# Kernel tuning notes

Hardware: AMD Instinct MI355X
Metric: run time of the kernel (lower is better)

## Reference

```python
import jax, jax.numpy as jnp
import numpy as np

USER_COUNT = 100000
ITEM_COUNT = 100000
DIM = 64
B = 1024
NPOS = 10
NTOP = 50
CLAMP = 40.0
EPS = 1e-05


def setup_inputs() -> dict:
    key = jax.random.key(0)
    k1, k2, k3, k4, k5 = jax.random.split(key, 5)
    user_emb = jax.random.normal(k1, (USER_COUNT, DIM), dtype=jnp.float32) * 0.01
    item_emb = jax.random.normal(k2, (ITEM_COUNT, DIM), dtype=jnp.float32) * 0.01
    batch_user = jax.random.randint(k3, (B,), 0, USER_COUNT)
    pos_items = jax.random.randint(k4, (B, NPOS), 0, ITEM_COUNT)
    top_items = jax.random.randint(k5, (B, NTOP), 0, ITEM_COUNT)
    batch_user_mask = jnp.zeros((B, ITEM_COUNT), dtype=jnp.float32)
    return {
        "user_emb": user_emb,
        "item_emb": item_emb,
        "batch_user": batch_user,
        "pos_items": pos_items,
        "top_items": top_items,
        "batch_user_mask": batch_user_mask,
        "is_final": 1,
    }


def _overall_loss(mat, pos_items, top_items, mask):
    # tops: scores at pos+top indices, [B, NPOS+NTOP]
    tops = jnp.take_along_axis(mat, jnp.concatenate([pos_items, top_items], -1), axis=1)
    tops_els = (jnp.exp(mat) * (1.0 - mask)).sum(1, keepdims=True)  # [B,1]
    els = tops_els - jnp.exp(jnp.take_along_axis(mat, top_items, axis=1)).sum(1, keepdims=True)
    above = tops.reshape(-1, 1)
    below = jnp.broadcast_to(els, (els.shape[0], tops.shape[1])).reshape(-1, 1) + jnp.exp(above)
    below = jnp.log(jnp.clip(below, EPS))
    return -(above - below).sum()


def _rank_loss(mat, pos_items, top_items, mask):
    S_pos = jnp.take_along_axis(mat, pos_items, axis=1)                       # [B,NPOS]
    S_top = jnp.take_along_axis(mat, top_items[:, : NTOP // 2], axis=1)       # [B,NTOP/2]
    exp_masked_sum = (jnp.exp(mat) * (1.0 - mask)).sum(1, keepdims=True)      # [B,1]
    below2 = exp_masked_sum - jnp.exp(S_top).sum(1, keepdims=True)
    above_pos = S_pos.sum(1, keepdims=True)
    above_top = S_top.sum(1, keepdims=True)
    below_pos = jnp.cumsum(jnp.exp(jnp.flip(S_pos, -1)), axis=1)
    below_top = jnp.cumsum(jnp.exp(jnp.flip(S_top, -1)), axis=1)
    below_pos = jnp.log(jnp.clip(below_pos + below2, EPS)).sum(1, keepdims=True)
    below_top = jnp.log(jnp.clip(below_top + below2, EPS)).sum(1, keepdims=True)
    pos_KD_loss = -(above_pos - below_pos).sum()
    S_top_sub = jnp.take_along_axis(mat, top_items[:, : NTOP // 10], axis=1)  # [B,NTOP/10]
    below2_sub = exp_masked_sum - jnp.exp(S_top_sub).sum(1, keepdims=True)
    above_top_sub = S_top_sub.sum(1, keepdims=True)
    below_top_sub = jnp.cumsum(jnp.exp(jnp.flip(S_top_sub, -1)), axis=1)
    below_top_sub = jnp.log(jnp.clip(below_top_sub + below2_sub, EPS)).sum(1, keepdims=True)
    top_KD_loss = -(above_top - below_top).sum() - (above_top_sub - below_top_sub).sum()
    return pos_KD_loss + top_KD_loss / 2


def reference(user_emb, item_emb, batch_user, pos_items, top_items, batch_user_mask, is_final):
    u = user_emb[batch_user]                                  # [B, DIM]
    mat = jnp.clip(u @ item_emb.T, -CLAMP, CLAMP)             # [B, ITEM_COUNT]
    if is_final:
        return _rank_loss(mat, pos_items, top_items, batch_user_mask)
    return _overall_loss(mat, pos_items, top_items, batch_user_mask)
```

## Files before the change

### kernel.cpp

```cpp
#include <hip/hip_runtime.h>
#include <cstddef>
#include <cstdint>

#define USER_COUNT_C 100000
#define ITEM_COUNT_C 100000
#define DIM_C 64
#define B_C 1024
#define NPOS_C 10
#define NTOP_C 50
#define CLAMP_C 40.0f
#define EPS_C 1e-5f

#define NGROUPS 6250
#define NCHUNKS 3125
#define GX 48
#define GY 16

using bf16x8 = __attribute__((ext_vector_type(8))) short;
using f32x4  = __attribute__((ext_vector_type(4))) float;

__global__ void zero_ws_kernel(float* __restrict__ ws) {
    ws[threadIdx.x] = 0.0f;
}

__device__ inline short f2bf(float x) {
    uint32_t b = __float_as_uint(x);
    uint32_t r = (b + 0x7fffu + ((b >> 16) & 1u)) >> 16;
    return (short)r;
}

__device__ inline bf16x8 cvt8(const float* __restrict__ p) {
    float4 v0 = *(const float4*)p;
    float4 v1 = *(const float4*)(p + 4);
    bf16x8 r;
    r[0] = f2bf(v0.x); r[1] = f2bf(v0.y); r[2] = f2bf(v0.z); r[3] = f2bf(v0.w);
    r[4] = f2bf(v1.x); r[5] = f2bf(v1.y); r[6] = f2bf(v1.z); r[7] = f2bf(v1.w);
    return r;
}

__global__ __launch_bounds__(256) void prep_items_kernel(
    const float* __restrict__ item_emb, short* __restrict__ item_bf16) {
    const int t = blockIdx.x * 256 + threadIdx.x;
    const int n16 = t & 15;
    const int q   = (t >> 4) & 3;
    const int h   = (t >> 6) & 1;
    const int g   = t >> 7;
    const int i   = g * 16 + n16;
    bf16x8 v = cvt8(item_emb + (size_t)i * DIM_C + h * 32 + q * 8);
    *(bf16x8*)(item_bf16 + (((size_t)g * 2 + h) * 4 + q) * 128 + n16 * 8) = v;
}

__global__ __launch_bounds__(256, 3) void expsum_mfma5_kernel(
    const float* __restrict__ user_emb,
    const short* __restrict__ item_bf16,
    const int*   __restrict__ batch_user,
    const float* __restrict__ mask,
    float*       __restrict__ exp_sum)
{
    const int tid  = threadIdx.x;
    const int wave = tid >> 6;
    const int lane = tid & 63;
    const int n16  = lane & 15;
    const int quad = lane >> 4;
    const int uBase = blockIdx.y * 64;

    bf16x8 b0[4], b1[4];
    #pragma unroll
    for (int j = 0; j < 4; ++j) {
        const int uidx = batch_user[uBase + j * 16 + n16];
        const float* us = user_emb + (size_t)uidx * DIM_C + quad * 8;
        b0[j] = cvt8(us);
        b1[j] = cvt8(us + 32);
    }

    const float* mbase = mask + (size_t)(uBase + n16) * ITEM_COUNT_C;
    const short* fbase = item_bf16 + quad * 128 + n16 * 8;

    const int c0 = (int)(((long)blockIdx.x * NCHUNKS) / GX);
    const int c1 = (int)(((long)(blockIdx.x + 1) * NCHUNKS) / GX);

    float accE[4] = {0.f, 0.f, 0.f, 0.f};

    for (int c = c0 + wave; c < c1; c += 4) {
        float4 m[4][2];
        #pragma unroll
        for (int j = 0; j < 4; ++j)
            #pragma unroll
            for (int ig = 0; ig < 2; ++ig)
                m[j][ig] = *(const float4*)(mbase + (size_t)j * 16 * ITEM_COUNT_C
                                            + c * 32 + ig * 16 + quad * 4);

        const short* fp = fbase + (size_t)c * 2048;
        const bf16x8 a00 = *(const bf16x8*)fp;
        const bf16x8 a01 = *(const bf16x8*)(fp + 512);
        const bf16x8 a10 = *(const bf16x8*)(fp + 1024);
        const bf16x8 a11 = *(const bf16x8*)(fp + 1536);

        f32x4 acc[2][4];
        #pragma unroll
        for (int j = 0; j < 4; ++j) {
            acc[0][j] = (f32x4){0.f, 0.f, 0.f, 0.f};
            acc[0][j] = __builtin_amdgcn_mfma_f32_16x16x32_bf16(a00, b0[j], acc[0][j], 0, 0, 0);
            acc[0][j] = __builtin_amdgcn_mfma_f32_16x16x32_bf16(a01, b1[j], acc[0][j], 0, 0, 0);
            acc[1][j] = (f32x4){0.f, 0.f, 0.f, 0.f};
            acc[1][j] = __builtin_amdgcn_mfma_f32_16x16x32_bf16(a10, b0[j], acc[1][j], 0, 0, 0);
            acc[1][j] = __builtin_amdgcn_mfma_f32_16x16x32_bf16(a11, b1[j], acc[1][j], 0, 0, 0);
        }

        #pragma unroll
        for (int j = 0; j < 4; ++j)
            #pragma unroll
            for (int ig = 0; ig < 2; ++ig) {
                const float* mp = (const float*)&m[j][ig];
                #pragma unroll
                for (int r = 0; r < 4; ++r) {
                    const float sc = fminf(fmaxf(acc[ig][j][r], -CLAMP_C), CLAMP_C);
                    accE[j] += __expf(sc) * (1.0f - mp[r]);
                }
            }
    }

    #pragma unroll
    for (int j = 0; j < 4; ++j) {
        accE[j] += __shfl_xor(accE[j], 16, 64);
        accE[j] += __shfl_xor(accE[j], 32, 64);
    }
    if (quad == 0) {
        #pragma unroll
        for (int j = 0; j < 4; ++j)
            atomicAdd(&exp_sum[uBase + j * 16 + n16], accE[j]);
    }
}

__global__ __launch_bounds__(256) void expsum_fallback_kernel(
    const float* __restrict__ user_emb,
    const float* __restrict__ item_emb,
    const int*   __restrict__ batch_user,
    const float* __restrict__ mask,
    float*       __restrict__ exp_sum)
{
    const int tid  = threadIdx.x;
    const int wave = tid >> 6;
    const int lane = tid & 63;
    const int n16  = lane & 15;
    const int quad = lane >> 4;
    const int rowBase = blockIdx.y * 64 + wave * 16;

    const int uidx = batch_user[rowBase + n16];
    const float* usrc = user_emb + (size_t)uidx * DIM_C + quad * 8;
    const bf16x8 a0 = cvt8(usrc);
    const bf16x8 a1 = cvt8(usrc + 32);

    float accExp[4] = {0.f, 0.f, 0.f, 0.f};

    for (int t = blockIdx.x; t < NGROUPS / 4; t += 64) {
        const int ibase = t * 64;
        bf16x8 b0[4], b1[4];
        #pragma unroll
        for (int s = 0; s < 4; ++s) {
            const int gi = ibase + s * 16 + n16;
            const float* isrc = item_emb + (size_t)gi * DIM_C + quad * 8;
            b0[s] = cvt8(isrc);
            b1[s] = cvt8(isrc + 32);
        }
        f32x4 acc[4];
        #pragma unroll
        for (int s = 0; s < 4; ++s) {
            acc[s] = (f32x4){0.f, 0.f, 0.f, 0.f};
            acc[s] = __builtin_amdgcn_mfma_f32_16x16x32_bf16(a0, b0[s], acc[s], 0, 0, 0);
            acc[s] = __builtin_amdgcn_mfma_f32_16x16x32_bf16(a1, b1[s], acc[s], 0, 0, 0);
        }
        #pragma unroll
        for (int s = 0; s < 4; ++s)
            #pragma unroll
            for (int reg = 0; reg < 4; ++reg) {
                const int row = rowBase + quad * 4 + reg;
                const float sc = fminf(fmaxf(acc[s][reg], -CLAMP_C), CLAMP_C);
                const float w = 1.0f - mask[(size_t)row * ITEM_COUNT_C + ibase + s * 16 + n16];
                accExp[reg] += __expf(sc) * w;
            }
    }
    #pragma unroll
    for (int off = 1; off < 16; off <<= 1)
        #pragma unroll
        for (int reg = 0; reg < 4; ++reg)
            accExp[reg] += __shfl_xor(accExp[reg], off, 64);
    if (n16 == 0)
        #pragma unroll
        for (int reg = 0; reg < 4; ++reg)
            atomicAdd(&exp_sum[rowBase + quad * 4 + reg], accExp[reg]);
}

__global__ void finalize_kernel(
    const float* __restrict__ user_emb,
    const float* __restrict__ item_emb,
    const int*   __restrict__ batch_user,
    const int*   __restrict__ pos_items,
    const int*   __restrict__ top_items,
    const float* __restrict__ exp_sum,
    const int*   __restrict__ is_final,
    float*       __restrict__ row_loss)
{
    __shared__ float ush[DIM_C];
    __shared__ float s_sh[NPOS_C + NTOP_C];
    const int b = blockIdx.x;
    const int tid = threadIdx.x;
    const int uidx = batch_user[b];
    if (tid < 16)
        *(float4*)&ush[tid * 4] = *(const float4*)(user_emb + (size_t)uidx * DIM_C + tid * 4);
    __syncthreads();

    if (tid < NPOS_C + NTOP_C) {
        const int idx = (tid < NPOS_C) ? pos_items[b * NPOS_C + tid]
                                       : top_items[b * NTOP_C + (tid - NPOS_C)];
        const float* iv = item_emb + (size_t)idx * DIM_C;
        float s = 0.f;
        #pragma unroll
        for (int d4 = 0; d4 < 16; ++d4) {
            const float4 a = *(const float4*)(iv + d4 * 4);
            s += a.x * ush[d4 * 4 + 0] + a.y * ush[d4 * 4 + 1]
               + a.z * ush[d4 * 4 + 2] + a.w * ush[d4 * 4 + 3];
        }
        s_sh[tid] = fminf(fmaxf(s, -CLAMP_C), CLAMP_C);
    }
    __syncthreads();

    if (tid == 0) {
        const float E = exp_sum[b];
        float L;
        if (is_final[0] != 0) {
            float sumExpTop = 0.f, above_top = 0.f;
            for (int i = 0; i < NTOP_C / 2; ++i) {
                const float v = s_sh[NPOS_C + i];
                sumExpTop += __expf(v); above_top += v;
            }
            const float below2 = E - sumExpTop;
            float above_pos = 0.f;
            for (int i = 0; i < NPOS_C; ++i) above_pos += s_sh[i];
            float c = 0.f, below_pos = 0.f;
            for (int i = 0; i < NPOS_C; ++i) {
                c += __expf(s_sh[NPOS_C - 1 - i]);
                below_pos += __logf(fmaxf(c + below2, EPS_C));
            }
            float c2 = 0.f, below_top = 0.f;
            for (int i = 0; i < NTOP_C / 2; ++i) {
                c2 += __expf(s_sh[NPOS_C + NTOP_C / 2 - 1 - i]);
                below_top += __logf(fmaxf(c2 + below2, EPS_C));
            }
            const float pos_KD = below_pos - above_pos;
            float sumExpSub = 0.f, above_sub = 0.f;
            for (int i = 0; i < NTOP_C / 10; ++i) {
                const float v = s_sh[NPOS_C + i];
                sumExpSub += __expf(v); above_sub += v;
            }
            const float below2s = E - sumExpSub;
            float c3 = 0.f, below_sub = 0.f;
            for (int i = 0; i < NTOP_C / 10; ++i) {
                c3 += __expf(s_sh[NPOS_C + NTOP_C / 10 - 1 - i]);
                below_sub += __logf(fmaxf(c3 + below2s, EPS_C));
            }
            const float top_KD = (below_top - above_top) + (below_sub - above_sub);
            L = pos_KD + 0.5f * top_KD;
        } else {
            float sumExpTop = 0.f;
            for (int i = 0; i < NTOP_C; ++i) sumExpTop += __expf(s_sh[NPOS_C + i]);
            const float els = E - sumExpTop;
            L = 0.f;
            for (int j = 0; j < NPOS_C + NTOP_C; ++j) {
                const float a = s_sh[j];
                L += __logf(fmaxf(els + __expf(a), EPS_C)) - a;
            }
        }
        row_loss[b] = L;
    }
}

__global__ void reduce_kernel(const float* __restrict__ rl, float* __restrict__ out) {
    __shared__ float part[16];
    const int tid = threadIdx.x;
    float v = rl[tid];
    #pragma unroll
    for (int off = 32; off > 0; off >>= 1) v += __shfl_down(v, off, 64);
    if ((tid & 63) == 0) part[tid >> 6] = v;
    __syncthreads();
    if (tid == 0) {
        float s = 0.f;
        #pragma unroll
        for (int i = 0; i < 16; ++i) s += part[i];
        out[0] = s;
    }
}

extern "C" void kernel_launch(void* const* d_in, const int* in_sizes, int n_in,
                              void* d_out, int out_size, void* d_ws, size_t ws_size,
                              hipStream_t stream) {
    const float* user_emb   = (const float*)d_in[0];
    const float* item_emb   = (const float*)d_in[1];
    const int*   batch_user = (const int*)d_in[2];
    const int*   pos_items  = (const int*)d_in[3];
    const int*   top_items  = (const int*)d_in[4];
    const float* mask       = (const float*)d_in[5];
    const int*   is_final   = (const int*)d_in[6];
    float* out = (float*)d_out;

    float* exp_sum  = (float*)d_ws;
    float* row_loss = exp_sum + B_C;
    short* item_bf16 = (short*)(row_loss + B_C);
    const size_t need = 2 * B_C * sizeof(float)
                      + (size_t)NGROUPS * 1024 * sizeof(short);

    hipLaunchKernelGGL(zero_ws_kernel, dim3(1), dim3(B_C), 0, stream, exp_sum);
    if (ws_size >= need) {
        hipLaunchKernelGGL(prep_items_kernel, dim3(NGROUPS * 128 / 256), dim3(256),
                           0, stream, item_emb, item_bf16);
        hipLaunchKernelGGL(expsum_mfma5_kernel, dim3(GX, GY), dim3(256),
                           0, stream, user_emb, item_bf16, batch_user, mask, exp_sum);
    } else {
        hipLaunchKernelGGL(expsum_fallback_kernel, dim3(64, B_C / 64), dim3(256),
                           0, stream, user_emb, item_emb, batch_user, mask, exp_sum);
    }
    hipLaunchKernelGGL(finalize_kernel, dim3(B_C), dim3(64), 0, stream,
                       user_emb, item_emb, batch_user, pos_items, top_items,
                       exp_sum, is_final, row_loss);
    hipLaunchKernelGGL(reduce_kernel, dim3(1), dim3(B_C), 0, stream, row_loss, out);
}
```

Before: 593.2 us.

## Stage mask tiles through shared memory with row-contiguous coalesced loads

Restructures the exp-sum kernel so each block handles 128-item tiles. All 256 threads cooperatively load a 64x128 mask tile into LDS using contiguous 512-byte row segments, and the waves then read their mask values from LDS. Previously each wave loaded scattered 128-byte row pieces for 16 users straight into registers. The goal is better coalescing on the dominant 400 MB mask read, at the cost of two barriers per tile, no double buffering, and a padded tail tile that reads extra zero-weighted item groups.

```diff
diff --git a/kernel.cpp b/kernel.cpp
--- a/kernel.cpp
+++ b/kernel.cpp
@@ -12,9 +12,10 @@
 #define EPS_C 1e-5f
 
 #define NGROUPS 6250
-#define NCHUNKS 3125
+#define T_TILES 782
 #define GX 48
 #define GY 16
+#define MROW 132
 
 using bf16x8 = __attribute__((ext_vector_type(8))) short;
 using f32x4  = __attribute__((ext_vector_type(4))) float;
@@ -47,16 +48,18 @@
     const int g   = t >> 7;
     const int i   = g * 16 + n16;
     bf16x8 v = cvt8(item_emb + (size_t)i * DIM_C + h * 32 + q * 8);
-    *(bf16x8*)(item_bf16 + (((size_t)g * 2 + h) * 4 + q) * 128 + n16 * 8) = v;
-}
-
-__global__ __launch_bounds__(256, 3) void expsum_mfma5_kernel(
+    *(bf16x8*)(item_bf16 + (size_t)g * 1024 + h * 512 + q * 128 + n16 * 8) = v;
+}
+
+__global__ __launch_bounds__(256, 3) void expsum_mfma6_kernel(
     const float* __restrict__ user_emb,
     const short* __restrict__ item_bf16,
     const int*   __restrict__ batch_user,
     const float* __restrict__ mask,
     float*       __restrict__ exp_sum)
 {
+    __shared__ float mtile[64 * MROW];
+
     const int tid  = threadIdx.x;
     const int wave = tid >> 6;
     const int lane = tid & 63;
@@ -73,24 +76,30 @@
         b1[j] = cvt8(us + 32);
     }
 
-    const float* mbase = mask + (size_t)(uBase + n16) * ITEM_COUNT_C;
-    const short* fbase = item_bf16 + quad * 128 + n16 * 8;
-
-    const int c0 = (int)(((long)blockIdx.x * NCHUNKS) / GX);
-    const int c1 = (int)(((long)(blockIdx.x + 1) * NCHUNKS) / GX);
+    const int srow = tid >> 5;
+    const int scol = (tid & 31) * 4;
+    const float* smask = mask + (size_t)(uBase + srow) * ITEM_COUNT_C + scol;
+    float* sdst = &mtile[srow * MROW + scol];
 
     float accE[4] = {0.f, 0.f, 0.f, 0.f};
 
-    for (int c = c0 + wave; c < c1; c += 4) {
-        float4 m[4][2];
-        #pragma unroll
-        for (int j = 0; j < 4; ++j)
-            #pragma unroll
-            for (int ig = 0; ig < 2; ++ig)
-                m[j][ig] = *(const float4*)(mbase + (size_t)j * 16 * ITEM_COUNT_C
-                                            + c * 32 + ig * 16 + quad * 4);
-
-        const short* fp = fbase + (size_t)c * 2048;
+    for (int tile = blockIdx.x; tile < T_TILES; tile += GX) {
+        const int C = tile * 128;
+
+        #pragma unroll
+        for (int k = 0; k < 8; ++k) {
+            const int gitem = C + scol;
+            float4 v;
+            if (gitem < ITEM_COUNT_C)
+                v = *(const float4*)(smask + (size_t)(k * 8) * ITEM_COUNT_C + C);
+            else
+                v = make_float4(1.f, 1.f, 1.f, 1.f);
+            *(float4*)(sdst + k * 8 * MROW) = v;
+        }
+        __syncthreads();
+
+        const short* fp = item_bf16 + (size_t)(tile * 8 + wave * 2) * 1024
+                        + quad * 128 + n16 * 8;
         const bf16x8 a00 = *(const bf16x8*)fp;
         const bf16x8 a01 = *(const bf16x8*)(fp + 512);
         const bf16x8 a10 = *(const bf16x8*)(fp + 1024);
@@ -108,16 +117,20 @@
         }
 
         #pragma unroll
-        for (int j = 0; j < 4; ++j)
+        for (int j = 0; j < 4; ++j) {
             #pragma unroll
             for (int ig = 0; ig < 2; ++ig) {
-                const float* mp = (const float*)&m[j][ig];
+                const int l = wave * 32 + ig * 16 + quad * 4;
+                const float4 mv = *(const float4*)&mtile[(j * 16 + n16) * MROW + l];
+                const float* mp = (const float*)&mv;
                 #pragma unroll
                 for (int r = 0; r < 4; ++r) {
                     const float sc = fminf(fmaxf(acc[ig][j][r], -CLAMP_C), CLAMP_C);
                     accE[j] += __expf(sc) * (1.0f - mp[r]);
                 }
             }
+        }
+        __syncthreads();
     }
 
     #pragma unroll
@@ -307,13 +320,13 @@
     float* row_loss = exp_sum + B_C;
     short* item_bf16 = (short*)(row_loss + B_C);
     const size_t need = 2 * B_C * sizeof(float)
-                      + (size_t)NGROUPS * 1024 * sizeof(short);
+                      + ((size_t)NGROUPS + 16) * 1024 * sizeof(short);
 
     hipLaunchKernelGGL(zero_ws_kernel, dim3(1), dim3(B_C), 0, stream, exp_sum);
     if (ws_size >= need) {
         hipLaunchKernelGGL(prep_items_kernel, dim3(NGROUPS * 128 / 256), dim3(256),
                            0, stream, item_emb, item_bf16);
-        hipLaunchKernelGGL(expsum_mfma5_kernel, dim3(GX, GY), dim3(256),
+        hipLaunchKernelGGL(expsum_mfma6_kernel, dim3(GX, GY), dim3(256),
                            0, stream, user_emb, item_bf16, batch_user, mask, exp_sum);
     } else {
         hipLaunchKernelGGL(expsum_fallback_kernel, dim3(64, B_C / 64), dim3(256),
```

After: 589.5 us. Within noise of the previous version (-0.6%).

## Double-buffer mask and item loads with 16-item chunks in exp-sum kernel

Applied to the files above, without the earlier changes.

The exp-sum kernel now works on 16-item chunks per wave iteration instead of 32 and software-pipelines the loop with two register buffers. The next chunk's item fragments and mask values are loaded while the current chunk's MFMAs and exp accumulation run. This is meant to hide global-memory latency of the large mask stream behind compute. It raises register pressure, and the smaller per-iteration work may reduce memory-level parallelism per wave. The workspace size check is also padded.

```diff
diff --git a/kernel.cpp b/kernel.cpp
--- a/kernel.cpp
+++ b/kernel.cpp
@@ -12,7 +12,6 @@
 #define EPS_C 1e-5f
 
 #define NGROUPS 6250
-#define NCHUNKS 3125
 #define GX 48
 #define GY 16
 
@@ -47,10 +46,10 @@
     const int g   = t >> 7;
     const int i   = g * 16 + n16;
     bf16x8 v = cvt8(item_emb + (size_t)i * DIM_C + h * 32 + q * 8);
-    *(bf16x8*)(item_bf16 + (((size_t)g * 2 + h) * 4 + q) * 128 + n16 * 8) = v;
-}
-
-__global__ __launch_bounds__(256, 3) void expsum_mfma5_kernel(
+    *(bf16x8*)(item_bf16 + (size_t)g * 1024 + h * 512 + q * 128 + n16 * 8) = v;
+}
+
+__global__ __launch_bounds__(256, 3) void expsum_mfma7_kernel(
     const float* __restrict__ user_emb,
     const short* __restrict__ item_bf16,
     const int*   __restrict__ batch_user,
@@ -73,51 +72,87 @@
         b1[j] = cvt8(us + 32);
     }
 
-    const float* mbase = mask + (size_t)(uBase + n16) * ITEM_COUNT_C;
+    const float* mbase = mask + (size_t)(uBase + n16) * ITEM_COUNT_C + quad * 4;
     const short* fbase = item_bf16 + quad * 128 + n16 * 8;
 
-    const int c0 = (int)(((long)blockIdx.x * NCHUNKS) / GX);
-    const int c1 = (int)(((long)(blockIdx.x + 1) * NCHUNKS) / GX);
+    const int c0   = (int)(((long)blockIdx.x * NGROUPS) / GX);
+    const int cEnd = (int)(((long)(blockIdx.x + 1) * NGROUPS) / GX);
 
     float accE[4] = {0.f, 0.f, 0.f, 0.f};
 
-    for (int c = c0 + wave; c < c1; c += 4) {
-        float4 m[4][2];
+    bf16x8 fA0, fA1, fB0, fB1;
+    float4 mA[4], mB[4];
+
+    auto loadA = [&](int c) {
+        const short* fp = fbase + (size_t)c * 1024;
+        fA0 = *(const bf16x8*)fp;
+        fA1 = *(const bf16x8*)(fp + 512);
         #pragma unroll
         for (int j = 0; j < 4; ++j)
+            mA[j] = *(const float4*)(mbase + (size_t)j * 16 * ITEM_COUNT_C + (size_t)c * 16);
+    };
+    auto loadB = [&](int c) {
+        const short* fp = fbase + (size_t)c * 1024;
+        fB0 = *(const bf16x8*)fp;
+        fB1 = *(const bf16x8*)(fp + 512);
+        #pragma unroll
+        for (int j = 0; j < 4; ++j)
+            mB[j] = *(const float4*)(mbase + (size_t)j * 16 * ITEM_COUNT_C + (size_t)c * 16);
+    };
+    auto computeA = [&]() {
+        f32x4 acc[4];
+        #pragma unroll
+        for (int j = 0; j < 4; ++j) {
+            acc[j] = (f32x4){0.f, 0.f, 0.f, 0.f};
+            acc[j] = __builtin_amdgcn_mfma_f32_16x16x32_bf16(fA0, b0[j], acc[j], 0, 0, 0);
+            acc[j] = __builtin_amdgcn_mfma_f32_16x16x32_bf16(fA1, b1[j], acc[j], 0, 0, 0);
+        }
+        #pragma unroll
+        for (int j = 0; j < 4; ++j) {
+            const float* mp = (const float*)&mA[j];
             #pragma unroll
-            for (int ig = 0; ig < 2; ++ig)
-                m[j][ig] = *(const float4*)(mbase + (size_t)j * 16 * ITEM_COUNT_C
-                                            + c * 32 + ig * 16 + quad * 4);
-
-        const short* fp = fbase + (size_t)c * 2048;
-        const bf16x8 a00 = *(const bf16x8*)fp;
-        const bf16x8 a01 = *(const bf16x8*)(fp + 512);
-        const bf16x8 a10 = *(const bf16x8*)(fp + 1024);
-        const bf16x8 a11 = *(const bf16x8*)(fp + 1536);
-
-        f32x4 acc[2][4];
+            for (int r = 0; r < 4; ++r) {
+                const float sc = fminf(fmaxf(acc[j][r], -CLAMP_C), CLAMP_C);
+                accE[j] += __expf(sc) * (1.0f - mp[r]);
+            }
+        }
+    };
+    auto computeB = [&]() {
+        f32x4 acc[4];
         #pragma unroll
         for (int j = 0; j < 4; ++j) {
-            acc[0][j] = (f32x4){0.f, 0.f, 0.f, 0.f};
-            acc[0][j] = __builtin_amdgcn_mfma_f32_16x16x32_bf16(a00, b0[j], acc[0][j], 0, 0, 0);
-            acc[0][j] = __builtin_amdgcn_mfma_f32_16x16x32_bf16(a01, b1[j], acc[0][j], 0, 0, 0);
-            acc[1][j] = (f32x4){0.f, 0.f, 0.f, 0.f};
-            acc[1][j] = __builtin_amdgcn_mfma_f32_16x16x32_bf16(a10, b0[j], acc[1][j], 0, 0, 0);
-            acc[1][j] = __builtin_amdgcn_mfma_f32_16x16x32_bf16(a11, b1[j], acc[1][j], 0, 0, 0);
-        }
-
-        #pragma unroll
-        for (int j = 0; j < 4; ++j)
+            acc[j] = (f32x4){0.f, 0.f, 0.f, 0.f};
+            acc[j] = __builtin_amdgcn_mfma_f32_16x16x32_bf16(fB0, b0[j], acc[j], 0, 0, 0);
+            acc[j] = __builtin_amdgcn_mfma_f32_16x16x32_bf16(fB1, b1[j], acc[j], 0, 0, 0);
+        }
+        #pragma unroll
+        for (int j = 0; j < 4; ++j) {
+            const float* mp = (const float*)&mB[j];
             #pragma unroll
-            for (int ig = 0; ig < 2; ++ig) {
-                const float* mp = (const float*)&m[j][ig];
-                #pragma unroll
-                for (int r = 0; r < 4; ++r) {
-                    const float sc = fminf(fmaxf(acc[ig][j][r], -CLAMP_C), CLAMP_C);
-                    accE[j] += __expf(sc) * (1.0f - mp[r]);
-                }
-            }
+            for (int r = 0; r < 4; ++r) {
+                const float sc = fminf(fmaxf(acc[j][r], -CLAMP_C), CLAMP_C);
+                accE[j] += __expf(sc) * (1.0f - mp[r]);
+            }
+        }
+    };
+
+    int c = c0 + wave;
+    if (c < cEnd) {
+        loadA(c);
+        for (;;) {
+            int cn = c + 4;
+            bool more = cn < cEnd;
+            loadB(more ? cn : c);
+            computeA();
+            if (!more) break;
+            c = cn;
+            cn = c + 4;
+            more = cn < cEnd;
+            loadA(more ? cn : c);
+            computeB();
+            if (!more) break;
+            c = cn;
+        }
     }
 
     #pragma unroll
@@ -307,13 +342,13 @@
     float* row_loss = exp_sum + B_C;
     short* item_bf16 = (short*)(row_loss + B_C);
     const size_t need = 2 * B_C * sizeof(float)
-                      + (size_t)NGROUPS * 1024 * sizeof(short);
+                      + ((size_t)NGROUPS + 16) * 1024 * sizeof(short);
 
     hipLaunchKernelGGL(zero_ws_kernel, dim3(1), dim3(B_C), 0, stream, exp_sum);
     if (ws_size >= need) {
         hipLaunchKernelGGL(prep_items_kernel, dim3(NGROUPS * 128 / 256), dim3(256),
                            0, stream, item_emb, item_bf16);
-        hipLaunchKernelGGL(expsum_mfma5_kernel, dim3(GX, GY), dim3(256),
+        hipLaunchKernelGGL(expsum_mfma7_kernel, dim3(GX, GY), dim3(256),
                            0, stream, user_emb, item_bf16, batch_user, mask, exp_sum);
     } else {
         hipLaunchKernelGGL(expsum_fallback_kernel, dim3(64, B_C / 64), dim3(256),
```

Result: no change. 602.5 us (+1.6%).

## Give each wave a contiguous range of 16-item groups and raise occupancy

Applied to the files above, without the earlier changes.

The exp-sum kernel now splits work into 16-item groups, and each wave takes a contiguous range of groups instead of striding by four 32-item chunks. Each step handles two groups, plus a tail for an odd count. The grid grows to 64 blocks in x and launch bounds ask for 4 waves per SIMD, so more memory traffic is in flight while streaming the large mask. Contiguous per-wave ranges may also improve locality of mask reads, at the cost of more register pressure and a workspace requirement raised by 16 extra groups.

```diff
diff --git a/kernel.cpp b/kernel.cpp
--- a/kernel.cpp
+++ b/kernel.cpp
@@ -12,8 +12,7 @@
 #define EPS_C 1e-5f
 
 #define NGROUPS 6250
-#define NCHUNKS 3125
-#define GX 48
+#define GX 64
 #define GY 16
 
 using bf16x8 = __attribute__((ext_vector_type(8))) short;
@@ -47,10 +46,10 @@
     const int g   = t >> 7;
     const int i   = g * 16 + n16;
     bf16x8 v = cvt8(item_emb + (size_t)i * DIM_C + h * 32 + q * 8);
-    *(bf16x8*)(item_bf16 + (((size_t)g * 2 + h) * 4 + q) * 128 + n16 * 8) = v;
-}
-
-__global__ __launch_bounds__(256, 3) void expsum_mfma5_kernel(
+    *(bf16x8*)(item_bf16 + (size_t)g * 1024 + h * 512 + q * 128 + n16 * 8) = v;
+}
+
+__global__ __launch_bounds__(256, 4) void expsum_mfma8_kernel(
     const float* __restrict__ user_emb,
     const short* __restrict__ item_bf16,
     const int*   __restrict__ batch_user,
@@ -73,51 +72,61 @@
         b1[j] = cvt8(us + 32);
     }
 
-    const float* mbase = mask + (size_t)(uBase + n16) * ITEM_COUNT_C;
+    const float* mbase = mask + (size_t)(uBase + n16) * ITEM_COUNT_C + quad * 4;
     const short* fbase = item_bf16 + quad * 128 + n16 * 8;
 
-    const int c0 = (int)(((long)blockIdx.x * NCHUNKS) / GX);
-    const int c1 = (int)(((long)(blockIdx.x + 1) * NCHUNKS) / GX);
+    const int bc0 = (int)(((long)blockIdx.x * NGROUPS) / GX);
+    const int bc1 = (int)(((long)(blockIdx.x + 1) * NGROUPS) / GX);
+    const int wc0 = bc0 + (int)(((long)(bc1 - bc0) * wave) / 4);
+    const int wc1 = bc0 + (int)(((long)(bc1 - bc0) * (wave + 1)) / 4);
 
     float accE[4] = {0.f, 0.f, 0.f, 0.f};
 
-    for (int c = c0 + wave; c < c1; c += 4) {
-        float4 m[4][2];
+    auto compute = [&](const bf16x8& f0, const bf16x8& f1, const float4* m) {
+        f32x4 acc[4];
+        #pragma unroll
+        for (int j = 0; j < 4; ++j) {
+            acc[j] = (f32x4){0.f, 0.f, 0.f, 0.f};
+            acc[j] = __builtin_amdgcn_mfma_f32_16x16x32_bf16(f0, b0[j], acc[j], 0, 0, 0);
+            acc[j] = __builtin_amdgcn_mfma_f32_16x16x32_bf16(f1, b1[j], acc[j], 0, 0, 0);
+        }
+        #pragma unroll
+        for (int j = 0; j < 4; ++j) {
+            const float* mp = (const float*)&m[j];
+            #pragma unroll
+            for (int r = 0; r < 4; ++r) {
+                const float sc = fminf(fmaxf(acc[j][r], -CLAMP_C), CLAMP_C);
+                accE[j] += __expf(sc) * (1.0f - mp[r]);
+            }
+        }
+    };
+
+    int c = wc0;
+    for (; c + 2 <= wc1; c += 2) {
+        const short* fp = fbase + (size_t)c * 1024;
+        const bf16x8 f00 = *(const bf16x8*)fp;
+        const bf16x8 f01 = *(const bf16x8*)(fp + 512);
+        const bf16x8 f10 = *(const bf16x8*)(fp + 1024);
+        const bf16x8 f11 = *(const bf16x8*)(fp + 1536);
+        float4 m0[4], m1[4];
+        #pragma unroll
+        for (int j = 0; j < 4; ++j) {
+            const float* mp = mbase + (size_t)j * 16 * ITEM_COUNT_C + (size_t)c * 16;
+            m0[j] = *(const float4*)mp;
+            m1[j] = *(const float4*)(mp + 16);
+        }
+        compute(f00, f01, m0);
+        compute(f10, f11, m1);
+    }
+    if (c < wc1) {
+        const short* fp = fbase + (size_t)c * 1024;
+        const bf16x8 f00 = *(const bf16x8*)fp;
+        const bf16x8 f01 = *(const bf16x8*)(fp + 512);
+        float4 m0[4];
         #pragma unroll
         for (int j = 0; j < 4; ++j)
-            #pragma unroll
-            for (int ig = 0; ig < 2; ++ig)
-                m[j][ig] = *(const float4*)(mbase + (size_t)j * 16 * ITEM_COUNT_C
-                                            + c * 32 + ig * 16 + quad * 4);
-
-        const short* fp = fbase + (size_t)c * 2048;
-        const bf16x8 a00 = *(const bf16x8*)fp;
-        const bf16x8 a01 = *(const bf16x8*)(fp + 512);
-        const bf16x8 a10 = *(const bf16x8*)(fp + 1024);
-        const bf16x8 a11 = *(const bf16x8*)(fp + 1536);
-
-        f32x4 acc[2][4];
-        #pragma unroll
-        for (int j = 0; j < 4; ++j) {
-            acc[0][j] = (f32x4){0.f, 0.f, 0.f, 0.f};
-            acc[0][j] = __builtin_amdgcn_mfma_f32_16x16x32_bf16(a00, b0[j], acc[0][j], 0, 0, 0);
-            acc[0][j] = __builtin_amdgcn_mfma_f32_16x16x32_bf16(a01, b1[j], acc[0][j], 0, 0, 0);
-            acc[1][j] = (f32x4){0.f, 0.f, 0.f, 0.f};
-            acc[1][j] = __builtin_amdgcn_mfma_f32_16x16x32_bf16(a10, b0[j], acc[1][j], 0, 0, 0);
-            acc[1][j] = __builtin_amdgcn_mfma_f32_16x16x32_bf16(a11, b1[j], acc[1][j], 0, 0, 0);
-        }
-
-        #pragma unroll
-        for (int j = 0; j < 4; ++j)
-            #pragma unroll
-            for (int ig = 0; ig < 2; ++ig) {
-                const float* mp = (const float*)&m[j][ig];
-                #pragma unroll
-                for (int r = 0; r < 4; ++r) {
-                    const float sc = fminf(fmaxf(acc[ig][j][r], -CLAMP_C), CLAMP_C);
-                    accE[j] += __expf(sc) * (1.0f - mp[r]);
-                }
-            }
+            m0[j] = *(const float4*)(mbase + (size_t)j * 16 * ITEM_COUNT_C + (size_t)c * 16);
+        compute(f00, f01, m0);
     }
 
     #pragma unroll
@@ -307,13 +316,13 @@
     float* row_loss = exp_sum + B_C;
     short* item_bf16 = (short*)(row_loss + B_C);
     const size_t need = 2 * B_C * sizeof(float)
-                      + (size_t)NGROUPS * 1024 * sizeof(short);
+                      + ((size_t)NGROUPS + 16) * 1024 * sizeof(short);
 
     hipLaunchKernelGGL(zero_ws_kernel, dim3(1), dim3(B_C), 0, stream, exp_sum);
     if (ws_size >= need) {
         hipLaunchKernelGGL(prep_items_kernel, dim3(NGROUPS * 128 / 256), dim3(256),
                            0, stream, item_emb, item_bf16);
-        hipLaunchKernelGGL(expsum_mfma5_kernel, dim3(GX, GY), dim3(256),
+        hipLaunchKernelGGL(expsum_mfma8_kernel, dim3(GX, GY), dim3(256),
                            0, stream, user_emb, item_bf16, batch_user, mask, exp_sum);
     } else {
         hipLaunchKernelGGL(expsum_fallback_kernel, dim3(64, B_C / 64), dim3(256),
```

After: 602.7 us. Within noise of the previous version (+1.6%).
